# Kernel optimization log

Measured on AMD Instinct MI355X. Metric: run time of the kernel, lower is better.

## Reference

```python
import jax, jax.numpy as jnp
import numpy as np

B, H_SP, W_SP = 16, 32, 32          # batch, spatial height/width (L = H*W = 1024)
EMBED, N_HEADS = 768, 24
HEAD_DIM = EMBED // N_HEADS          # 32
L = H_SP * W_SP


def make_so2_matrices(h, w, head_dim):
    """Per-position SO(2) rotation matrices, shape (h*w, head_dim//2, 2, 2).

    Faithful to GTAttention._init_so2_matrices: 2D integer coords, RoPE-style
    log-spaced frequencies, matrices stacked per (coord_dim, freq) then
    flattened and truncated to head_dim//2 2x2 blocks.
    """
    n_freqs = head_dim // 4 + (1 if head_dim % 4 != 0 else 0)
    yy, xx = jnp.meshgrid(jnp.arange(h, dtype=jnp.float32),
                          jnp.arange(w, dtype=jnp.float32), indexing='ij')
    coord = jnp.stack([yy, xx], axis=-1)                       # (h, w, 2)
    freqs = 10000.0 ** (-jnp.arange(n_freqs, dtype=jnp.float32) / n_freqs)
    theta = coord[..., :, None] * freqs                        # (h, w, 2, nf)
    c, s = jnp.cos(theta), jnp.sin(theta)
    row0 = jnp.stack([c, -s], axis=-1)
    row1 = jnp.stack([s, c], axis=-1)
    mats = jnp.stack([row0, row1], axis=-2)                    # (h, w, 2, nf, 2, 2)
    mats = mats.reshape(h * w, 2 * n_freqs, 2, 2)[:, : head_dim // 2]
    return mats                                                # (L, head_dim//2, 2, 2)


def apply_group_action(mat, x):
    """mat: (L, D/2, 2, 2); x: (B, H, L, D) -> rotated x, same shape."""
    b, h, l, d = x.shape
    x2 = x.reshape(b, h, l, d // 2, 2)
    y = jnp.einsum('lfij,bhlfj->bhlfi', mat, x2)
    return y.reshape(b, h, l, d)


def setup_inputs() -> dict:
    key = jax.random.key(0)
    ks = jax.random.split(key, 5)
    scale = 1.0 / np.sqrt(EMBED)
    x = jax.random.normal(ks[0], (B, L, EMBED), dtype=jnp.float32)
    W_qkv = jax.random.normal(ks[1], (3 * EMBED, EMBED), dtype=jnp.float32) * scale
    b_qkv = jnp.zeros((3 * EMBED,), dtype=jnp.float32)
    W_o = jax.random.normal(ks[2], (EMBED, EMBED), dtype=jnp.float32) * scale
    b_o = jnp.zeros((EMBED,), dtype=jnp.float32)
    base = make_so2_matrices(H_SP, W_SP, HEAD_DIM)
    return {
        'x': x, 'W_qkv': W_qkv, 'b_qkv': b_qkv, 'W_o': W_o, 'b_o': b_o,
        'mat_q': base, 'mat_k': base, 'mat_v': base,
        'mat_o': jnp.swapaxes(base, -2, -1),
    }


def reference(x, W_qkv, b_qkv, W_o, b_o, mat_q, mat_k, mat_v, mat_o):
    b, l, _ = x.shape
    qkv = x @ W_qkv.T + b_qkv                                   # (B, L, 3E)
    q, k, v = jnp.split(qkv, 3, axis=-1)
    def heads(t):  # (B, L, E) -> (B, H, L, D)
        return t.reshape(b, l, N_HEADS, HEAD_DIM).transpose(0, 2, 1, 3)
    q, k, v = heads(q), heads(k), heads(v)
    # GTA: learnable SO(2) rotations on q, k, v
    q = apply_group_action(mat_q, q)
    k = apply_group_action(mat_k, k)
    v = apply_group_action(mat_v, v)
    # scaled dot-product attention
    scores = jnp.einsum('bhqd,bhkd->bhqk', q, k) / np.sqrt(HEAD_DIM)
    attn = jax.nn.softmax(scores, axis=-1)
    out = jnp.einsum('bhqk,bhkd->bhqd', attn, v)
    # inverse (transposed) rotation on the output
    out = apply_group_action(mat_o, out)
    out = out.transpose(0, 2, 1, 3).reshape(b, l, EMBED)
    return out @ W_o.T + b_o
```

## Files before the change

### kernel.cpp

```cpp
#include <hip/hip_runtime.h>
#include <cstdint>
#include <cstddef>
#include <math.h>

typedef __attribute__((ext_vector_type(8))) short short8;
typedef __attribute__((ext_vector_type(4))) float f32x4;
typedef __attribute__((ext_vector_type(4))) unsigned short u16x4;
typedef unsigned short u16;
typedef unsigned int u32;

#define DEVI static __device__ __forceinline__

DEVI float bf2f(u16 u){ union{u32 i; float f;} v; v.i = ((u32)u)<<16; return v.f; }
DEVI u16 f2bf(float x){ union{u32 i; float f;} v; v.f = x; u32 r = v.i + 0x7FFFu + ((v.i>>16)&1u); return (u16)(r>>16); }

DEVI void gload16(const void* g, void* l){
  __builtin_amdgcn_global_load_lds((__attribute__((address_space(1))) void*)g,
                                   (__attribute__((address_space(3))) void*)l, 16, 0, 0);
}

__global__ __launch_bounds__(256)
void conv_f2b(const f32x4* __restrict__ s, u16x4* __restrict__ d, int n4)
{
  for (int i = blockIdx.x*blockDim.x + threadIdx.x; i < n4; i += gridDim.x*blockDim.x){
    const f32x4 v = s[i];
    u16x4 o;
    o[0] = f2bf(v[0]); o[1] = f2bf(v[1]); o[2] = f2bf(v[2]); o[3] = f2bf(v[3]);
    d[i] = o;
  }
}

template<int NDIM, int EPI>
__global__ __launch_bounds__(256, 2)
void gta_gemm(const u16* __restrict__ A, const u16* __restrict__ B,
              const float* __restrict__ bias,
              u16* __restrict__ O0, u16* __restrict__ O1, u16* __restrict__ O2,
              float* __restrict__ OF,
              const float* __restrict__ MQ, const float* __restrict__ MK,
              const float* __restrict__ MV)
{
  constexpr int KD = 768;
  constexpr int NBN = NDIM / 128;
  constexpr int NT = KD / 32;
  __shared__ u16 As[2][128*32];
  __shared__ u16 Bs[2][128*32];

  const int tid = threadIdx.x;
  const int nwg = gridDim.x;
  const int cpx = nwg >> 3;
  const int bid = blockIdx.x;
  const int swz = (bid & 7)*cpx + (bid >> 3);
  const int bm = swz / NBN, bn = swz % NBN;

  const int lane = tid & 63, w = tid >> 6;
  const int g = lane >> 4, c = lane & 15;
  const int wr = w >> 1, wc = w & 1;

  const u16* aSrc[2]; const u16* bSrc[2]; int dOff[2];
  #pragma unroll
  for (int i=0;i<2;i++){
    const int cl = i*256 + tid;
    const int row = cl >> 2, cpos = cl & 3;
    aSrc[i] = A + (size_t)(bm*128+row)*KD + cpos*8;
    bSrc[i] = B + (size_t)(bn*128+row)*KD + cpos*8;
    dOff[i] = (i*256 + (tid & ~63))*16;
  }

  auto stage = [&](int buf, int kt){
    #pragma unroll
    for (int i=0;i<2;i++){
      gload16(aSrc[i] + kt*32, (char*)(&As[buf][0]) + dOff[i]);
      gload16(bSrc[i] + kt*32, (char*)(&Bs[buf][0]) + dOff[i]);
    }
  };

  f32x4 acc[4][4] = {};

  stage(0, 0);
  __syncthreads();
  int cur = 0;
  for (int kt=0; kt<NT; ++kt){
    if (kt+1 < NT) stage(cur^1, kt+1);
    const char* ab = (const char*)&As[cur][0];
    const char* bb = (const char*)&Bs[cur][0];
    short8 af[4], bf[4];
    #pragma unroll
    for (int mi=0;mi<4;mi++) af[mi] = *(const short8*)(ab + (wr*64 + mi*16 + c)*64 + g*16);
    #pragma unroll
    for (int ni=0;ni<4;ni++) bf[ni] = *(const short8*)(bb + (wc*64 + ni*16 + c)*64 + g*16);
    #pragma unroll
    for (int mi=0;mi<4;mi++)
      #pragma unroll
      for (int ni=0;ni<4;ni++)
        acc[mi][ni] = __builtin_amdgcn_mfma_f32_16x16x32_bf16(af[mi], bf[ni], acc[mi][ni], 0,0,0);
    __syncthreads();
    cur ^= 1;
  }

  if constexpr (EPI == 0){
    #pragma unroll
    for (int ni=0; ni<4; ni++){
      const int n = bn*128 + wc*64 + ni*16 + c;
      const float bv = bias[n];
      const int X = n / 768;
      const int nn = n - X*768;
      const int h = nn >> 5, d = nn & 31;
      const int fi = d >> 1, r = d & 1;
      const float* mp = (X==0) ? MQ : ((X==1) ? MK : MV);
      const float qs = (X==0) ? 0.17677669529663687f : 1.0f;
      u16* dst01 = (X==0) ? O0 : O1;
      #pragma unroll
      for (int mi=0; mi<4; mi++){
        #pragma unroll
        for (int j=0; j<4; j++){
          const int m = bm*128 + wr*64 + mi*16 + g*4 + j;
          const int l = m & 1023, bix = m >> 10;
          const float val = acc[mi][ni][j] + bv;
          const float oth = __shfl_xor(val, 1);
          const float2 mrow = *(const float2*)(mp + (size_t)l*64 + fi*4 + r*2);
          const float x0 = r ? oth : val;
          const float x1 = r ? val : oth;
          const float y = (mrow.x*x0 + mrow.y*x1) * qs;
          const int head = bix*24 + h;
          if (X == 2) O2[(size_t)(head*32 + d)*1024 + l] = f2bf(y);
          else        dst01[((size_t)head*1024 + l)*32 + d] = f2bf(y);
        }
      }
    }
  } else {
    #pragma unroll
    for (int ni=0; ni<4; ni++){
      const int n = bn*128 + wc*64 + ni*16 + c;
      const float bv = bias[n];
      #pragma unroll
      for (int mi=0; mi<4; mi++){
        const int mb = bm*128 + wr*64 + mi*16 + g*4;
        #pragma unroll
        for (int j=0; j<4; j++)
          OF[(size_t)(mb+j)*NDIM + n] = acc[mi][ni][j] + bv;
      }
    }
  }
}

__global__ __launch_bounds__(256, 2)
void gta_attn(const u16* __restrict__ Qm, const u16* __restrict__ Km,
              const u16* __restrict__ Vt, const float* __restrict__ MO,
              u16* __restrict__ AO)
{
  const int tid = threadIdx.x;
  const int bid = blockIdx.x;
  const int nwg = gridDim.x;
  const int cpx = nwg >> 3;
  const int swz = (bid & 7)*cpx + (bid >> 3);
  const int head = swz >> 3, qb = swz & 7;

  const int lane = tid & 63, w = tid >> 6;
  const int g = lane >> 4, c = lane & 15;

  const u16* qh = Qm + (size_t)head*32768;
  const u16* kh = Km + (size_t)head*32768;
  const u16* vh = Vt + (size_t)head*32768;

  short8 qf[2];
  #pragma unroll
  for (int i=0;i<2;i++){
    const int qrow = qb*128 + w*32 + i*16 + c;
    qf[i] = *(const short8*)(qh + (size_t)qrow*32 + g*8);
  }

  f32x4 acc[2][2] = {};
  float mrun[2] = {-INFINITY, -INFINITY};
  float lrun[2] = {0.f, 0.f};
  const f32x4 fz = {0.f, 0.f, 0.f, 0.f};

  for (int t=0; t<32; ++t){
    const int kv0 = t*32;
    const short8 ka0 = *(const short8*)(kh + (size_t)(kv0 + c)*32 + g*8);
    const short8 ka1 = *(const short8*)(kh + (size_t)(kv0 + 16 + c)*32 + g*8);
    short8 pb[2];
    #pragma unroll
    for (int db=0; db<2; ++db){
      const int d = db*16 + c;
      const u16* vrow = vh + (size_t)d*1024 + kv0;
      const u32* lo = (const u32*)(vrow + 4*g);
      const u32* hi = (const u32*)(vrow + 16 + 4*g);
      union{u32 u[4]; short8 s;} uu;
      uu.u[0]=lo[0]; uu.u[1]=lo[1]; uu.u[2]=hi[0]; uu.u[3]=hi[1];
      pb[db]=uu.s;
    }
    #pragma unroll
    for (int qi=0; qi<2; ++qi){
      const f32x4 s0 = __builtin_amdgcn_mfma_f32_16x16x32_bf16(ka0, qf[qi], fz, 0,0,0);
      const f32x4 s1 = __builtin_amdgcn_mfma_f32_16x16x32_bf16(ka1, qf[qi], fz, 0,0,0);
      float mt = fmaxf(fmaxf(fmaxf(s0[0],s0[1]),fmaxf(s0[2],s0[3])),
                       fmaxf(fmaxf(s1[0],s1[1]),fmaxf(s1[2],s1[3])));
      mt = fmaxf(mt, __shfl_xor(mt, 16));
      mt = fmaxf(mt, __shfl_xor(mt, 32));
      const float mnew = fmaxf(mrun[qi], mt);
      const float sc = __expf(mrun[qi] - mnew);
      mrun[qi] = mnew;
      const float p0 = __expf(s0[0]-mnew), p1 = __expf(s0[1]-mnew);
      const float p2 = __expf(s0[2]-mnew), p3 = __expf(s0[3]-mnew);
      const float p4 = __expf(s1[0]-mnew), p5 = __expf(s1[1]-mnew);
      const float p6 = __expf(s1[2]-mnew), p7 = __expf(s1[3]-mnew);
      lrun[qi] = lrun[qi]*sc + (((p0+p1)+(p2+p3)) + ((p4+p5)+(p6+p7)));
      short8 pa;
      pa[0]=(short)f2bf(p0); pa[1]=(short)f2bf(p1);
      pa[2]=(short)f2bf(p2); pa[3]=(short)f2bf(p3);
      pa[4]=(short)f2bf(p4); pa[5]=(short)f2bf(p5);
      pa[6]=(short)f2bf(p6); pa[7]=(short)f2bf(p7);
      const int gb = g*4;
      const float sb0 = __shfl(sc, gb+0), sb1 = __shfl(sc, gb+1);
      const float sb2 = __shfl(sc, gb+2), sb3 = __shfl(sc, gb+3);
      #pragma unroll
      for (int db=0; db<2; ++db){
        f32x4 a = acc[qi][db];
        a[0]*=sb0; a[1]*=sb1; a[2]*=sb2; a[3]*=sb3;
        acc[qi][db] = __builtin_amdgcn_mfma_f32_16x16x32_bf16(pa, pb[db], a, 0,0,0);
      }
    }
  }

  const int bix = head / 24, hh = head - bix*24;
  #pragma unroll
  for (int qi=0; qi<2; ++qi){
    float lt = lrun[qi];
    lt += __shfl_xor(lt, 16);
    lt += __shfl_xor(lt, 32);
    const float linv = 1.0f / lt;
    const int gb = g*4;
    const float lb[4] = { __shfl(linv, gb+0), __shfl(linv, gb+1),
                          __shfl(linv, gb+2), __shfl(linv, gb+3) };
    #pragma unroll
    for (int db=0; db<2; ++db){
      const int dh = db*16 + c;
      const int r = dh & 1, fi = dh >> 1;
      #pragma unroll
      for (int j=0; j<4; ++j){
        const float o = acc[qi][db][j] * lb[j];
        const float oth = __shfl_xor(o, 1);
        const int lseq = qb*128 + w*32 + qi*16 + gb + j;
        const float2 mrow = *(const float2*)(MO + (size_t)lseq*64 + fi*4 + r*2);
        const float y = mrow.x*(r ? oth : o) + mrow.y*(r ? o : oth);
        AO[((size_t)(bix*1024 + lseq))*768 + hh*32 + dh] = f2bf(y);
      }
    }
  }
}

extern "C" void kernel_launch(void* const* d_in, const int* in_sizes, int n_in,
                              void* d_out, int out_size, void* d_ws, size_t ws_size,
                              hipStream_t stream)
{
  (void)in_sizes; (void)n_in; (void)out_size; (void)ws_size;
  const float* x    = (const float*)d_in[0];
  const float* Wqkv = (const float*)d_in[1];
  const float* bqkv = (const float*)d_in[2];
  const float* Wo   = (const float*)d_in[3];
  const float* bo   = (const float*)d_in[4];
  const float* mq   = (const float*)d_in[5];
  const float* mk   = (const float*)d_in[6];
  const float* mv   = (const float*)d_in[7];
  const float* mo   = (const float*)d_in[8];
  float* out = (float*)d_out;

  const size_t NX   = (size_t)16*1024*768;
  const size_t NWQ  = (size_t)2304*768;
  const size_t NWO  = (size_t)768*768;
  const size_t SQ   = (size_t)384*1024*32;

  u16* xb   = (u16*)d_ws;
  u16* wqb  = xb  + NX;
  u16* wob  = wqb + NWQ;
  u16* q_l  = wob + NWO;
  u16* k_l  = q_l + SQ;
  u16* vT   = k_l + SQ;
  u16* ao   = xb;

  hipLaunchKernelGGL(conv_f2b, dim3(2048), dim3(256), 0, stream,
                     (const f32x4*)x, (u16x4*)xb, (int)(NX/4));
  hipLaunchKernelGGL(conv_f2b, dim3(1024), dim3(256), 0, stream,
                     (const f32x4*)Wqkv, (u16x4*)wqb, (int)(NWQ/4));
  hipLaunchKernelGGL(conv_f2b, dim3(512), dim3(256), 0, stream,
                     (const f32x4*)Wo, (u16x4*)wob, (int)(NWO/4));

  hipLaunchKernelGGL((gta_gemm<2304,0>), dim3(2304), dim3(256), 0, stream,
                     xb, wqb, bqkv, q_l, k_l, vT, (float*)nullptr, mq, mk, mv);
  hipLaunchKernelGGL(gta_attn, dim3(3072), dim3(256), 0, stream,
                     q_l, k_l, vT, mo, ao);
  hipLaunchKernelGGL((gta_gemm<768,1>), dim3(768), dim3(256), 0, stream,
                     ao, wob, bo, (u16*)nullptr, (u16*)nullptr, (u16*)nullptr, out,
                     (const float*)nullptr, (const float*)nullptr, (const float*)nullptr);
}
```

Measured before the change: 522.8 us.

## Prefetch next K/V tile, use exp2 with folded log2e, skip unchanged-max rescale

```diff
diff --git a/kernel.cpp b/kernel.cpp
--- a/kernel.cpp
+++ b/kernel.cpp
@@ -10,6 +10,12 @@
 typedef unsigned int u32;
 
 #define DEVI static __device__ __forceinline__
+
+#if __has_builtin(__builtin_amdgcn_exp2f)
+#define EXP2(x) __builtin_amdgcn_exp2f(x)
+#else
+#define EXP2(x) exp2f(x)
+#endif
 
 DEVI float bf2f(u16 u){ union{u32 i; float f;} v; v.i = ((u32)u)<<16; return v.f; }
 DEVI u16 f2bf(float x){ union{u32 i; float f;} v; v.f = x; u32 r = v.i + 0x7FFFu + ((v.i>>16)&1u); return (u16)(r>>16); }
@@ -107,7 +113,7 @@
       const int h = nn >> 5, d = nn & 31;
       const int fi = d >> 1, r = d & 1;
       const float* mp = (X==0) ? MQ : ((X==1) ? MK : MV);
-      const float qs = (X==0) ? 0.17677669529663687f : 1.0f;
+      const float qs = (X==0) ? 0.2550348663f : 1.0f;
       u16* dst01 = (X==0) ? O0 : O1;
       #pragma unroll
       for (int mi=0; mi<4; mi++){
@@ -169,16 +175,11 @@
     qf[i] = *(const short8*)(qh + (size_t)qrow*32 + g*8);
   }
 
-  f32x4 acc[2][2] = {};
-  float mrun[2] = {-INFINITY, -INFINITY};
-  float lrun[2] = {0.f, 0.f};
-  const f32x4 fz = {0.f, 0.f, 0.f, 0.f};
-
-  for (int t=0; t<32; ++t){
-    const int kv0 = t*32;
-    const short8 ka0 = *(const short8*)(kh + (size_t)(kv0 + c)*32 + g*8);
-    const short8 ka1 = *(const short8*)(kh + (size_t)(kv0 + 16 + c)*32 + g*8);
-    short8 pb[2];
+  auto loadK = [&](int kv0, short8& a0, short8& a1){
+    a0 = *(const short8*)(kh + (size_t)(kv0 + c)*32 + g*8);
+    a1 = *(const short8*)(kh + (size_t)(kv0 + 16 + c)*32 + g*8);
+  };
+  auto loadV = [&](int kv0, short8& b0, short8& b1){
     #pragma unroll
     for (int db=0; db<2; ++db){
       const int d = db*16 + c;
@@ -187,39 +188,62 @@
       const u32* hi = (const u32*)(vrow + 16 + 4*g);
       union{u32 u[4]; short8 s;} uu;
       uu.u[0]=lo[0]; uu.u[1]=lo[1]; uu.u[2]=hi[0]; uu.u[3]=hi[1];
-      pb[db]=uu.s;
-    }
+      if (db) b1 = uu.s; else b0 = uu.s;
+    }
+  };
+
+  f32x4 acc[2][2] = {};
+  float mrun[2] = {-INFINITY, -INFINITY};
+  float lrun[2] = {0.f, 0.f};
+  const f32x4 fz = {0.f, 0.f, 0.f, 0.f};
+
+  short8 kc0, kc1, vc0, vc1;
+  loadK(0, kc0, kc1);
+  loadV(0, vc0, vc1);
+
+  for (int t=0; t<32; ++t){
+    const int nxt = ((t+1) & 31) * 32;
+    short8 kn0, kn1, vn0, vn1;
+    loadK(nxt, kn0, kn1);
+    loadV(nxt, vn0, vn1);
+
     #pragma unroll
     for (int qi=0; qi<2; ++qi){
-      const f32x4 s0 = __builtin_amdgcn_mfma_f32_16x16x32_bf16(ka0, qf[qi], fz, 0,0,0);
-      const f32x4 s1 = __builtin_amdgcn_mfma_f32_16x16x32_bf16(ka1, qf[qi], fz, 0,0,0);
-      float mt = fmaxf(fmaxf(fmaxf(s0[0],s0[1]),fmaxf(s0[2],s0[3])),
-                       fmaxf(fmaxf(s1[0],s1[1]),fmaxf(s1[2],s1[3])));
-      mt = fmaxf(mt, __shfl_xor(mt, 16));
-      mt = fmaxf(mt, __shfl_xor(mt, 32));
-      const float mnew = fmaxf(mrun[qi], mt);
-      const float sc = __expf(mrun[qi] - mnew);
-      mrun[qi] = mnew;
-      const float p0 = __expf(s0[0]-mnew), p1 = __expf(s0[1]-mnew);
-      const float p2 = __expf(s0[2]-mnew), p3 = __expf(s0[3]-mnew);
-      const float p4 = __expf(s1[0]-mnew), p5 = __expf(s1[1]-mnew);
-      const float p6 = __expf(s1[2]-mnew), p7 = __expf(s1[3]-mnew);
-      lrun[qi] = lrun[qi]*sc + (((p0+p1)+(p2+p3)) + ((p4+p5)+(p6+p7)));
+      const f32x4 s0 = __builtin_amdgcn_mfma_f32_16x16x32_bf16(kc0, qf[qi], fz, 0,0,0);
+      const f32x4 s1 = __builtin_amdgcn_mfma_f32_16x16x32_bf16(kc1, qf[qi], fz, 0,0,0);
+      const float mt8 = fmaxf(fmaxf(fmaxf(s0[0],s0[1]),fmaxf(s0[2],s0[3])),
+                              fmaxf(fmaxf(s1[0],s1[1]),fmaxf(s1[2],s1[3])));
+      if (__any(mt8 > mrun[qi])) {
+        float mt = fmaxf(mt8, __shfl_xor(mt8, 16));
+        mt = fmaxf(mt, __shfl_xor(mt, 32));
+        const float mnew = fmaxf(mrun[qi], mt);
+        const float sc = EXP2(mrun[qi] - mnew);
+        mrun[qi] = mnew;
+        lrun[qi] *= sc;
+        const int gb = g*4;
+        const float sb0 = __shfl(sc, gb+0), sb1 = __shfl(sc, gb+1);
+        const float sb2 = __shfl(sc, gb+2), sb3 = __shfl(sc, gb+3);
+        #pragma unroll
+        for (int db=0; db<2; ++db){
+          acc[qi][db][0]*=sb0; acc[qi][db][1]*=sb1;
+          acc[qi][db][2]*=sb2; acc[qi][db][3]*=sb3;
+        }
+      }
+      const float m = mrun[qi];
+      const float p0 = EXP2(s0[0]-m), p1 = EXP2(s0[1]-m);
+      const float p2 = EXP2(s0[2]-m), p3 = EXP2(s0[3]-m);
+      const float p4 = EXP2(s1[0]-m), p5 = EXP2(s1[1]-m);
+      const float p6 = EXP2(s1[2]-m), p7 = EXP2(s1[3]-m);
+      lrun[qi] += (((p0+p1)+(p2+p3)) + ((p4+p5)+(p6+p7)));
       short8 pa;
       pa[0]=(short)f2bf(p0); pa[1]=(short)f2bf(p1);
       pa[2]=(short)f2bf(p2); pa[3]=(short)f2bf(p3);
       pa[4]=(short)f2bf(p4); pa[5]=(short)f2bf(p5);
       pa[6]=(short)f2bf(p6); pa[7]=(short)f2bf(p7);
-      const int gb = g*4;
-      const float sb0 = __shfl(sc, gb+0), sb1 = __shfl(sc, gb+1);
-      const float sb2 = __shfl(sc, gb+2), sb3 = __shfl(sc, gb+3);
-      #pragma unroll
-      for (int db=0; db<2; ++db){
-        f32x4 a = acc[qi][db];
-        a[0]*=sb0; a[1]*=sb1; a[2]*=sb2; a[3]*=sb3;
-        acc[qi][db] = __builtin_amdgcn_mfma_f32_16x16x32_bf16(pa, pb[db], a, 0,0,0);
-      }
-    }
+      acc[qi][0] = __builtin_amdgcn_mfma_f32_16x16x32_bf16(pa, vc0, acc[qi][0], 0,0,0);
+      acc[qi][1] = __builtin_amdgcn_mfma_f32_16x16x32_bf16(pa, vc1, acc[qi][1], 0,0,0);
+    }
+    kc0=kn0; kc1=kn1; vc0=vn0; vc1=vn1;
   }
 
   const int bix = head / 24, hh = head - bix*24;
```

After: 516.9 us. About the same (-1.1%).
